# Kernel optimization log

Hardware: AMD Instinct MI355X
Metric: run time of the kernel (lower is better)

Reference implementation:

```python
import jax, jax.numpy as jnp
import numpy as np

NUM_HEADS = 8  # matches init_kwargs

def setup_inputs() -> dict:
    key = jax.random.key(0)
    ks = jax.random.split(key, 5)
    b, n, c = 8, 4096, 512
    scale_in = 1.0 / np.sqrt(c)
    return {
        'x': jax.random.normal(ks[0], (b, n, c), jnp.float32),
        'wqkv_w': jax.random.normal(ks[1], (3 * c, c), jnp.float32) * scale_in,
        'wqkv_b': jax.random.normal(ks[2], (3 * c,), jnp.float32) * 0.02,
        'wp_w': jax.random.normal(ks[3], (c, c), jnp.float32) * scale_in,
        'wp_b': jax.random.normal(ks[4], (c,), jnp.float32) * 0.02,
    }

def reference(x, wqkv_w, wqkv_b, wp_w, wp_b):
    b, n, c = x.shape
    h = NUM_HEADS
    d = c // h
    # QKV projection (torch Linear: x @ W^T + b)
    qkv = x @ wqkv_w.T + wqkv_b                      # (b, n, 3c)
    qkv = jnp.transpose(qkv.reshape(b, n, 3, c), (2, 0, 1, 3))
    q, k, v = qkv[0], qkv[1], qkv[2]                 # each (b, n, c)
    # Faithful to original: reshape (b,n,h,d) -> (b,h,n,d) is a FLAT
    # reinterpretation (torch .reshape), not a transpose.
    q = q.reshape(b, n, h, d).reshape(b, h, n, d)
    k = k.reshape(b, n, h, d).reshape(b, h, n, d)
    v = v.reshape(b, n, h, d).reshape(b, h, n, d)
    # Channel (cross-covariance) attention: contract over tokens n.
    scores = jnp.einsum('bhnd,bhne->bhde', q, k) / jnp.sqrt(jnp.float32(d))
    weights = jax.nn.softmax(scores, axis=-1)        # softmax over head_dim
    y = jnp.einsum('bhde,bhme->bhdm', weights, v)    # (b, h, d, n)
    y = jnp.transpose(y, (0, 3, 1, 2)).reshape(b, n, c)
    return y @ wp_w.T + wp_b
```

## Files before the change

kernel.cpp:

```cpp
#include <hip/hip_runtime.h>

typedef short s16x8 __attribute__((ext_vector_type(8)));
typedef float f32x4 __attribute__((ext_vector_type(4)));
typedef unsigned short us;

__device__ inline us f2bf(float f){
    union{float f;unsigned u;} v{f};
    unsigned r = v.u + 0x7fff + ((v.u>>16)&1);
    return (us)(r>>16);
}
__device__ inline float bf2f(us h){
    union{unsigned u;float f;} v{(unsigned)h<<16};
    return v.f;
}

__device__ __forceinline__ void glds16(const us* g, us* l){
    __builtin_amdgcn_global_load_lds(
        (const __attribute__((address_space(1))) unsigned int*)(g),
        (__attribute__((address_space(3))) unsigned int*)(l), 16, 0, 0);
}

__global__ void cast_f32_bf16(const float* __restrict__ src, us* __restrict__ dst, int n4){
    int i = blockIdx.x*blockDim.x + threadIdx.x;
    if(i < n4){
        float4 f = ((const float4*)src)[i];
        ushort4 o;
        o.x = f2bf(f.x); o.y = f2bf(f.y); o.z = f2bf(f.z); o.w = f2bf(f.w);
        ((ushort4*)dst)[i] = o;
    }
}

__launch_bounds__(256,2)
__global__ void gemm_qkv(const float* __restrict__ X, const us* __restrict__ B,
                         const float* __restrict__ bias, us* __restrict__ C){
    __shared__ __attribute__((aligned(16))) us sA[128*32];
    __shared__ __attribute__((aligned(16))) us sB[128*32];
    int t = threadIdx.x;
    int id = blockIdx.x;
    int xcd = id & 7, s = id >> 3;
    int nt = s % 12, mt = xcd*32 + s/12;
    int lane = t&63, wave = t>>6, quad = lane>>4, l15 = lane&15;
    int wm = wave>>1, wn = wave&1;

    int srA = t>>1, scA = (t&1)*16;
    const float* Ag = X + (size_t)(mt*128 + srA)*512 + scA;
    us* sAd = &sA[srA*32 + scA];

    int srB = wave*32 + (lane>>2), scB = (lane&3)*8;
    const us* Bg = B + (size_t)(nt*128 + srB)*512 + scB;
    us* sBw = &sB[(wave*32)*32];

    f32x4 acc[4][4];
    #pragma unroll
    for(int i=0;i<4;i++)
        #pragma unroll
        for(int j=0;j<4;j++) acc[i][j] = (f32x4){0.f,0.f,0.f,0.f};

    float4 p0 = ((const float4*)Ag)[0], p1 = ((const float4*)Ag)[1],
           p2 = ((const float4*)Ag)[2], p3 = ((const float4*)Ag)[3];

    for(int ki=0; ki<16; ki++){
        int k0 = ki*32;
        glds16(Bg + k0,          sBw);
        glds16(Bg + 16*512 + k0, sBw + 16*32);
        union{uint4 u[2]; us h[16];} o;
        o.h[0]=f2bf(p0.x); o.h[1]=f2bf(p0.y); o.h[2]=f2bf(p0.z); o.h[3]=f2bf(p0.w);
        o.h[4]=f2bf(p1.x); o.h[5]=f2bf(p1.y); o.h[6]=f2bf(p1.z); o.h[7]=f2bf(p1.w);
        o.h[8]=f2bf(p2.x); o.h[9]=f2bf(p2.y); o.h[10]=f2bf(p2.z); o.h[11]=f2bf(p2.w);
        o.h[12]=f2bf(p3.x); o.h[13]=f2bf(p3.y); o.h[14]=f2bf(p3.z); o.h[15]=f2bf(p3.w);
        *(uint4*)sAd = o.u[0]; *(uint4*)(sAd+8) = o.u[1];
        if(ki<15){
            const float4* nxt = (const float4*)(Ag + k0 + 32);
            p0 = nxt[0]; p1 = nxt[1]; p2 = nxt[2]; p3 = nxt[3];
        }
        __syncthreads();
        s16x8 af[4], bfr[4];
        #pragma unroll
        for(int i=0;i<4;i++) af[i]  = *(const s16x8*)&sA[(wm*64 + i*16 + l15)*32 + quad*8];
        #pragma unroll
        for(int j=0;j<4;j++) bfr[j] = *(const s16x8*)&sB[(wn*64 + j*16 + l15)*32 + quad*8];
        #pragma unroll
        for(int i=0;i<4;i++)
            #pragma unroll
            for(int j=0;j<4;j++)
                acc[i][j] = __builtin_amdgcn_mfma_f32_16x16x32_bf16(af[i], bfr[j], acc[i][j], 0,0,0);
        __syncthreads();
    }

    int row0 = mt*128 + wm*64, col0 = nt*128 + wn*64;
    #pragma unroll
    for(int j=0;j<4;j++){
        int col = col0 + j*16 + l15;
        float bv = bias[col];
        #pragma unroll
        for(int i=0;i<4;i++){
            int rbase = row0 + i*16 + quad*4;
            #pragma unroll
            for(int r=0;r<4;r++)
                C[(size_t)(rbase+r)*1536 + col] = f2bf(acc[i][j][r] + bv);
        }
    }
}

__launch_bounds__(256,2)
__global__ void attn_scores_mfma(const us* __restrict__ qkv, float* __restrict__ Sp){
    __shared__ __attribute__((aligned(16))) us sQt[64*64];
    __shared__ __attribute__((aligned(16))) us sKt[64*64];
    int t = threadIdx.x;
    int kb = blockIdx.x, head = blockIdx.y;
    int lane = t & 63, w = t >> 6;
    int quad = lane >> 4, l15 = lane & 15;

    f32x4 acc[4];
    #pragma unroll
    for(int j=0;j<4;j++) acc[j] = (f32x4){0.f,0.f,0.f,0.f};

    for(int chunk=0; chunk<8; chunk++){
        int r0 = head*512 + kb*64 + chunk*8;
        #pragma unroll
        for(int it=0; it<2; it++){
            int i = it*256 + t;
            int row8 = i>>6, l = i&63;
            int d0 = (l&7)*8;
            int off = ((row8 ^ (l&7))<<3) | (l>>3);
            const us* gq = qkv + (size_t)(r0+row8)*1536 + l*8;
            union{uint4 v; us s[8];} q, k;
            q.v = *(const uint4*)gq;
            k.v = *(const uint4*)(gq + 512);
            #pragma unroll
            for(int j=0;j<8;j++){
                sQt[(d0+j)*64 + off] = q.s[j];
                sKt[(d0+j)*64 + off] = k.s[j];
            }
        }
        __syncthreads();
        #pragma unroll
        for(int ks=0; ks<2; ks++){
            int d = w*16 + l15;
            int tb = ks*4 + quad;
            s16x8 af = *(const s16x8*)&sQt[d*64 + ((tb ^ (d>>3))<<3)];
            #pragma unroll
            for(int jt=0; jt<4; jt++){
                int e = jt*16 + l15;
                s16x8 bfv = *(const s16x8*)&sKt[e*64 + ((tb ^ (e>>3))<<3)];
                acc[jt] = __builtin_amdgcn_mfma_f32_16x16x32_bf16(af, bfv, acc[jt], 0,0,0);
            }
        }
        __syncthreads();
    }

    float* S = Sp + (size_t)(kb*64 + head)*4096;
    #pragma unroll
    for(int jt=0; jt<4; jt++){
        int e = jt*16 + l15;
        #pragma unroll
        for(int r=0; r<4; r++){
            int d = w*16 + quad*4 + r;
            S[d*64 + e] = acc[jt][r];
        }
    }
}

__global__ void softmax_fuse(const float* __restrict__ Sp, us* __restrict__ W){
    int head = blockIdx.x;
    int t = threadIdx.x;
    int d = t>>2, eg = (t&3)*16;
    float v[16];
    #pragma unroll
    for(int e=0;e<16;e++) v[e]=0.f;
    for(int kb=0; kb<8; kb++){
        const float* p = Sp + (size_t)(kb*64 + head)*4096 + d*64 + eg;
        #pragma unroll
        for(int e4=0;e4<4;e4++){
            float4 f = ((const float4*)p)[e4];
            v[e4*4+0]+=f.x; v[e4*4+1]+=f.y; v[e4*4+2]+=f.z; v[e4*4+3]+=f.w;
        }
    }
    float m = -1e30f;
    #pragma unroll
    for(int e=0;e<16;e++){ v[e] *= 0.125f; m = fmaxf(m, v[e]); }
    m = fmaxf(m, __shfl_xor(m, 1));
    m = fmaxf(m, __shfl_xor(m, 2));
    float s = 0.f;
    #pragma unroll
    for(int e=0;e<16;e++){ v[e] = __expf(v[e]-m); s += v[e]; }
    s += __shfl_xor(s, 1);
    s += __shfl_xor(s, 2);
    float inv = 1.f/s;
    union{uint4 u[2]; us h[16];} o;
    #pragma unroll
    for(int e=0;e<16;e++) o.h[e] = f2bf(v[e]*inv);
    uint4* wp = (uint4*)(W + (size_t)head*4096 + d*64 + eg);
    wp[0] = o.u[0]; wp[1] = o.u[1];
}

__launch_bounds__(256,1)
__global__ void wpfold(const us* __restrict__ wpbf, const us* __restrict__ W,
                       us* __restrict__ Mcat){
    __shared__ us sWt[64*72];
    int t = threadIdx.x;
    int head = blockIdx.x, b = head>>3, h = head&7;
    int lane = t&63, w = t>>6, quad = lane>>4, l15 = lane&15;
    #pragma unroll
    for(int it=0; it<2; it++){
        int idx = it*2048 + t*8;
        int d = idx>>6, e0 = idx&63;
        union{uint4 v; us s[8];} q;
        q.v = *(const uint4*)&W[(size_t)head*4096 + idx];
        #pragma unroll
        for(int j=0;j<8;j++) sWt[(e0+j)*72 + d] = q.s[j];
    }
    __syncthreads();
    #pragma unroll
    for(int i=0;i<8;i++){
        int nO = w*128 + i*16 + l15;
        s16x8 af0 = *(const s16x8*)&wpbf[(size_t)nO*512 + h*64 + quad*8];
        s16x8 af1 = *(const s16x8*)&wpbf[(size_t)nO*512 + h*64 + 32 + quad*8];
        #pragma unroll
        for(int j=0;j<4;j++){
            s16x8 bf0 = *(const s16x8*)&sWt[(j*16+l15)*72 + quad*8];
            s16x8 bf1 = *(const s16x8*)&sWt[(j*16+l15)*72 + 32 + quad*8];
            f32x4 acc = (f32x4){0.f,0.f,0.f,0.f};
            acc = __builtin_amdgcn_mfma_f32_16x16x32_bf16(af0, bf0, acc, 0,0,0);
            acc = __builtin_amdgcn_mfma_f32_16x16x32_bf16(af1, bf1, acc, 0,0,0);
            #pragma unroll
            for(int r=0;r<4;r++){
                int row = w*128 + i*16 + quad*4 + r;
                Mcat[((size_t)(b*512 + row))*512 + h*64 + j*16 + l15] = f2bf(acc[r]);
            }
        }
    }
}

__launch_bounds__(256,2)
__global__ void gemm_vout(const us* __restrict__ qkv, const us* __restrict__ Mcat,
                          const float* __restrict__ bias, float* __restrict__ out){
    __shared__ __attribute__((aligned(16))) us sA[128*32];
    __shared__ __attribute__((aligned(16))) us sB[128*32];
    int t = threadIdx.x;
    int id = blockIdx.x;
    int xcd = id & 7, s = id >> 3;
    int nt = s & 3, mt = xcd*32 + (s>>2);
    int b = mt>>5, mr = mt&31;
    int lane = t&63, wave = t>>6, quad = lane>>4, l15 = lane&15;
    int wm = wave>>1, wn = wave&1;

    int r = wave*32 + (lane>>2);
    int m = mr*128 + r;
    const us* Abase = qkv + ((size_t)(8*b)*512 + (m>>3))*1536 + 1024 + (m&7)*64 + (lane&3)*8;
    us* sAw = &sA[(wave*32)*32];

    int srB = wave*32 + (lane>>2), scB = (lane&3)*8;
    const us* Bg = Mcat + ((size_t)(b*512 + nt*128 + srB))*512 + scB;
    us* sBw = &sB[(wave*32)*32];

    f32x4 acc[4][4];
    #pragma unroll
    for(int i=0;i<4;i++)
        #pragma unroll
        for(int j=0;j<4;j++) acc[i][j] = (f32x4){0.f,0.f,0.f,0.f};

    for(int ki=0; ki<16; ki++){
        int k0 = ki*32;
        int h = k0>>6, e0 = k0&63;
        const us* Ag = Abase + (size_t)h*512*1536 + e0;
        glds16(Ag,            sAw);
        glds16(Ag + 2*1536,   sAw + 16*32);
        glds16(Bg + k0,           sBw);
        glds16(Bg + 16*512 + k0,  sBw + 16*32);
        __syncthreads();
        s16x8 af[4], bfr[4];
        #pragma unroll
        for(int i=0;i<4;i++) af[i]  = *(const s16x8*)&sA[(wm*64 + i*16 + l15)*32 + quad*8];
        #pragma unroll
        for(int j=0;j<4;j++) bfr[j] = *(const s16x8*)&sB[(wn*64 + j*16 + l15)*32 + quad*8];
        #pragma unroll
        for(int i=0;i<4;i++)
            #pragma unroll
            for(int j=0;j<4;j++)
                acc[i][j] = __builtin_amdgcn_mfma_f32_16x16x32_bf16(af[i], bfr[j], acc[i][j], 0,0,0);
        __syncthreads();
    }

    int row0 = b*4096 + mr*128 + wm*64;
    int col0 = nt*128 + wn*64;
    #pragma unroll
    for(int j=0;j<4;j++){
        int col = col0 + j*16 + l15;
        float bv = bias[col];
        #pragma unroll
        for(int i=0;i<4;i++){
            int rbase = row0 + i*16 + quad*4;
            #pragma unroll
            for(int r2=0;r2<4;r2++)
                out[(size_t)(rbase+r2)*512 + col] = acc[i][j][r2] + bv;
        }
    }
}

extern "C" void kernel_launch(void* const* d_in, const int* in_sizes, int n_in,
                              void* d_out, int out_size, void* d_ws, size_t ws_size,
                              hipStream_t stream){
    const float* x      = (const float*)d_in[0];
    const float* wqkv_w = (const float*)d_in[1];
    const float* wqkv_b = (const float*)d_in[2];
    const float* wp_w   = (const float*)d_in[3];
    const float* wp_b   = (const float*)d_in[4];

    char* ws = (char*)d_ws;
    us*    qkvbf  = (us*)(ws);
    float* Spart  = (float*)(ws + 100663296);
    us*    Wsm    = (us*)(ws + 109051904);
    us*    Mcat   = (us*)(ws + 109576192);
    us*    wqkvbf = (us*)(ws + 113770496);
    us*    wpbf   = (us*)(ws + 115343360);

    cast_f32_bf16<<<768, 256,0,stream>>>(wqkv_w, wqkvbf, 786432/4);
    cast_f32_bf16<<<256, 256,0,stream>>>(wp_w,   wpbf,   262144/4);

    gemm_qkv<<<3072,256,0,stream>>>(x, wqkvbf, wqkv_b, qkvbf);

    attn_scores_mfma<<<dim3(8,64),256,0,stream>>>(qkvbf, Spart);
    softmax_fuse<<<64,256,0,stream>>>(Spart, Wsm);

    wpfold<<<64,256,0,stream>>>(wpbf, Wsm, Mcat);

    gemm_vout<<<1024,256,0,stream>>>(qkvbf, Mcat, wp_b, (float*)d_out);
}
```

Before: 275.4 us.

## Pre-cast x to bf16, fuse softmax into fold, restage attention LDS loads

Adds a separate cast of x to bf16 so the QKV GEMM can stage both operands with direct global-to-LDS loads instead of converting fp32 in registers. Merges the two weight casts into one launch and folds the softmax kernel into the Wp-fold kernel, which removes a launch and the intermediate weights buffer. The score kernel's transposed LDS staging now uses padded rows with packed 32-bit stores in place of the XOR swizzle, and its occupancy bound is raised. In exchange it adds an extra pass over x (a read of fp32 and a write of bf16) through global memory.

```diff
diff --git a/kernel.cpp b/kernel.cpp
--- a/kernel.cpp
+++ b/kernel.cpp
@@ -9,10 +9,6 @@
     unsigned r = v.u + 0x7fff + ((v.u>>16)&1);
     return (us)(r>>16);
 }
-__device__ inline float bf2f(us h){
-    union{unsigned u;float f;} v{(unsigned)h<<16};
-    return v.f;
-}
 
 __device__ __forceinline__ void glds16(const us* g, us* l){
     __builtin_amdgcn_global_load_lds(
@@ -20,7 +16,7 @@
         (__attribute__((address_space(3))) unsigned int*)(l), 16, 0, 0);
 }
 
-__global__ void cast_f32_bf16(const float* __restrict__ src, us* __restrict__ dst, int n4){
+__global__ void cast_x(const float* __restrict__ src, us* __restrict__ dst, int n4){
     int i = blockIdx.x*blockDim.x + threadIdx.x;
     if(i < n4){
         float4 f = ((const float4*)src)[i];
@@ -30,8 +26,20 @@
     }
 }
 
+__global__ void cast_w(const float* __restrict__ wqkv_w, const float* __restrict__ wp_w,
+                       us* __restrict__ wqkvbf, us* __restrict__ wpbf){
+    int i = blockIdx.x*blockDim.x + threadIdx.x;
+    const float* s; us* d; int j;
+    if(i < 196608){ s = wqkv_w; d = wqkvbf; j = i; }
+    else          { s = wp_w;   d = wpbf;   j = i - 196608; }
+    float4 f = ((const float4*)s)[j];
+    ushort4 o;
+    o.x = f2bf(f.x); o.y = f2bf(f.y); o.z = f2bf(f.z); o.w = f2bf(f.w);
+    ((ushort4*)d)[j] = o;
+}
+
 __launch_bounds__(256,2)
-__global__ void gemm_qkv(const float* __restrict__ X, const us* __restrict__ B,
+__global__ void gemm_qkv(const us* __restrict__ A, const us* __restrict__ B,
                          const float* __restrict__ bias, us* __restrict__ C){
     __shared__ __attribute__((aligned(16))) us sA[128*32];
     __shared__ __attribute__((aligned(16))) us sB[128*32];
@@ -42,12 +50,11 @@
     int lane = t&63, wave = t>>6, quad = lane>>4, l15 = lane&15;
     int wm = wave>>1, wn = wave&1;
 
-    int srA = t>>1, scA = (t&1)*16;
-    const float* Ag = X + (size_t)(mt*128 + srA)*512 + scA;
-    us* sAd = &sA[srA*32 + scA];
-
-    int srB = wave*32 + (lane>>2), scB = (lane&3)*8;
-    const us* Bg = B + (size_t)(nt*128 + srB)*512 + scB;
+    int srow = wave*32 + (lane>>2);
+    int scol = (lane&3)*8;
+    const us* Ag = A + (size_t)(mt*128 + srow)*512 + scol;
+    const us* Bg = B + (size_t)(nt*128 + srow)*512 + scol;
+    us* sAw = &sA[(wave*32)*32];
     us* sBw = &sB[(wave*32)*32];
 
     f32x4 acc[4][4];
@@ -56,23 +63,11 @@
         #pragma unroll
         for(int j=0;j<4;j++) acc[i][j] = (f32x4){0.f,0.f,0.f,0.f};
 
-    float4 p0 = ((const float4*)Ag)[0], p1 = ((const float4*)Ag)[1],
-           p2 = ((const float4*)Ag)[2], p3 = ((const float4*)Ag)[3];
-
-    for(int ki=0; ki<16; ki++){
-        int k0 = ki*32;
+    for(int k0=0; k0<512; k0+=32){
+        glds16(Ag + k0,          sAw);
+        glds16(Ag + 16*512 + k0, sAw + 16*32);
         glds16(Bg + k0,          sBw);
         glds16(Bg + 16*512 + k0, sBw + 16*32);
-        union{uint4 u[2]; us h[16];} o;
-        o.h[0]=f2bf(p0.x); o.h[1]=f2bf(p0.y); o.h[2]=f2bf(p0.z); o.h[3]=f2bf(p0.w);
-        o.h[4]=f2bf(p1.x); o.h[5]=f2bf(p1.y); o.h[6]=f2bf(p1.z); o.h[7]=f2bf(p1.w);
-        o.h[8]=f2bf(p2.x); o.h[9]=f2bf(p2.y); o.h[10]=f2bf(p2.z); o.h[11]=f2bf(p2.w);
-        o.h[12]=f2bf(p3.x); o.h[13]=f2bf(p3.y); o.h[14]=f2bf(p3.z); o.h[15]=f2bf(p3.w);
-        *(uint4*)sAd = o.u[0]; *(uint4*)(sAd+8) = o.u[1];
-        if(ki<15){
-            const float4* nxt = (const float4*)(Ag + k0 + 32);
-            p0 = nxt[0]; p1 = nxt[1]; p2 = nxt[2]; p3 = nxt[3];
-        }
         __syncthreads();
         s16x8 af[4], bfr[4];
         #pragma unroll
@@ -102,14 +97,16 @@
     }
 }
 
-__launch_bounds__(256,2)
+__launch_bounds__(256,4)
 __global__ void attn_scores_mfma(const us* __restrict__ qkv, float* __restrict__ Sp){
-    __shared__ __attribute__((aligned(16))) us sQt[64*64];
-    __shared__ __attribute__((aligned(16))) us sKt[64*64];
+    __shared__ __attribute__((aligned(16))) us sQt[64*72];
+    __shared__ __attribute__((aligned(16))) us sKt[64*72];
     int t = threadIdx.x;
     int kb = blockIdx.x, head = blockIdx.y;
     int lane = t & 63, w = t >> 6;
     int quad = lane >> 4, l15 = lane & 15;
+    int p = t & 31;
+    int d0 = (t >> 5) * 8;
 
     f32x4 acc[4];
     #pragma unroll
@@ -117,32 +114,25 @@
 
     for(int chunk=0; chunk<8; chunk++){
         int r0 = head*512 + kb*64 + chunk*8;
-        #pragma unroll
-        for(int it=0; it<2; it++){
-            int i = it*256 + t;
-            int row8 = i>>6, l = i&63;
-            int d0 = (l&7)*8;
-            int off = ((row8 ^ (l&7))<<3) | (l>>3);
-            const us* gq = qkv + (size_t)(r0+row8)*1536 + l*8;
-            union{uint4 v; us s[8];} q, k;
-            q.v = *(const uint4*)gq;
-            k.v = *(const uint4*)(gq + 512);
-            #pragma unroll
-            for(int j=0;j<8;j++){
-                sQt[(d0+j)*64 + off] = q.s[j];
-                sKt[(d0+j)*64 + off] = k.s[j];
-            }
-        }
-        __syncthreads();
+        const us* g = qkv + (size_t)(r0 + (p>>2))*1536 + (2*(p&3))*64 + d0;
+        union{uint4 v; us h[8];} q0, q1, k0, k1;
+        q0.v = *(const uint4*)g;         q1.v = *(const uint4*)(g + 64);
+        k0.v = *(const uint4*)(g + 512); k1.v = *(const uint4*)(g + 576);
+        #pragma unroll
+        for(int j=0;j<8;j++){
+            *(unsigned*)&sQt[(d0+j)*72 + 2*p] = (unsigned)q0.h[j] | ((unsigned)q1.h[j]<<16);
+            *(unsigned*)&sKt[(d0+j)*72 + 2*p] = (unsigned)k0.h[j] | ((unsigned)k1.h[j]<<16);
+        }
+        __syncthreads();
+        int d = w*16 + l15;
         #pragma unroll
         for(int ks=0; ks<2; ks++){
-            int d = w*16 + l15;
             int tb = ks*4 + quad;
-            s16x8 af = *(const s16x8*)&sQt[d*64 + ((tb ^ (d>>3))<<3)];
+            s16x8 af = *(const s16x8*)&sQt[d*72 + tb*8];
             #pragma unroll
             for(int jt=0; jt<4; jt++){
                 int e = jt*16 + l15;
-                s16x8 bfv = *(const s16x8*)&sKt[e*64 + ((tb ^ (e>>3))<<3)];
+                s16x8 bfv = *(const s16x8*)&sKt[e*72 + tb*8];
                 acc[jt] = __builtin_amdgcn_mfma_f32_16x16x32_bf16(af, bfv, acc[jt], 0,0,0);
             }
         }
@@ -161,56 +151,43 @@
     }
 }
 
-__global__ void softmax_fuse(const float* __restrict__ Sp, us* __restrict__ W){
-    int head = blockIdx.x;
-    int t = threadIdx.x;
-    int d = t>>2, eg = (t&3)*16;
-    float v[16];
-    #pragma unroll
-    for(int e=0;e<16;e++) v[e]=0.f;
-    for(int kb=0; kb<8; kb++){
-        const float* p = Sp + (size_t)(kb*64 + head)*4096 + d*64 + eg;
-        #pragma unroll
-        for(int e4=0;e4<4;e4++){
-            float4 f = ((const float4*)p)[e4];
-            v[e4*4+0]+=f.x; v[e4*4+1]+=f.y; v[e4*4+2]+=f.z; v[e4*4+3]+=f.w;
-        }
-    }
-    float m = -1e30f;
-    #pragma unroll
-    for(int e=0;e<16;e++){ v[e] *= 0.125f; m = fmaxf(m, v[e]); }
-    m = fmaxf(m, __shfl_xor(m, 1));
-    m = fmaxf(m, __shfl_xor(m, 2));
-    float s = 0.f;
-    #pragma unroll
-    for(int e=0;e<16;e++){ v[e] = __expf(v[e]-m); s += v[e]; }
-    s += __shfl_xor(s, 1);
-    s += __shfl_xor(s, 2);
-    float inv = 1.f/s;
-    union{uint4 u[2]; us h[16];} o;
-    #pragma unroll
-    for(int e=0;e<16;e++) o.h[e] = f2bf(v[e]*inv);
-    uint4* wp = (uint4*)(W + (size_t)head*4096 + d*64 + eg);
-    wp[0] = o.u[0]; wp[1] = o.u[1];
-}
-
 __launch_bounds__(256,1)
-__global__ void wpfold(const us* __restrict__ wpbf, const us* __restrict__ W,
+__global__ void smfold(const float* __restrict__ Sp, const us* __restrict__ wpbf,
                        us* __restrict__ Mcat){
     __shared__ us sWt[64*72];
     int t = threadIdx.x;
     int head = blockIdx.x, b = head>>3, h = head&7;
     int lane = t&63, w = t>>6, quad = lane>>4, l15 = lane&15;
-    #pragma unroll
-    for(int it=0; it<2; it++){
-        int idx = it*2048 + t*8;
-        int d = idx>>6, e0 = idx&63;
-        union{uint4 v; us s[8];} q;
-        q.v = *(const uint4*)&W[(size_t)head*4096 + idx];
-        #pragma unroll
-        for(int j=0;j<8;j++) sWt[(e0+j)*72 + d] = q.s[j];
+
+    {
+        int d = t>>2, eg = (t&3)*16;
+        float v[16];
+        #pragma unroll
+        for(int e=0;e<16;e++) v[e]=0.f;
+        for(int kb=0; kb<8; kb++){
+            const float* pp = Sp + (size_t)(kb*64 + head)*4096 + d*64 + eg;
+            #pragma unroll
+            for(int e4=0;e4<4;e4++){
+                float4 f = ((const float4*)pp)[e4];
+                v[e4*4+0]+=f.x; v[e4*4+1]+=f.y; v[e4*4+2]+=f.z; v[e4*4+3]+=f.w;
+            }
+        }
+        float m = -1e30f;
+        #pragma unroll
+        for(int e=0;e<16;e++){ v[e] *= 0.125f; m = fmaxf(m, v[e]); }
+        m = fmaxf(m, __shfl_xor(m, 1));
+        m = fmaxf(m, __shfl_xor(m, 2));
+        float s = 0.f;
+        #pragma unroll
+        for(int e=0;e<16;e++){ v[e] = __expf(v[e]-m); s += v[e]; }
+        s += __shfl_xor(s, 1);
+        s += __shfl_xor(s, 2);
+        float inv = 1.f/s;
+        #pragma unroll
+        for(int e=0;e<16;e++) sWt[(eg+e)*72 + d] = f2bf(v[e]*inv);
     }
     __syncthreads();
+
     #pragma unroll
     for(int i=0;i<8;i++){
         int nO = w*128 + i*16 + l15;
@@ -309,21 +286,20 @@
 
     char* ws = (char*)d_ws;
     us*    qkvbf  = (us*)(ws);
-    float* Spart  = (float*)(ws + 100663296);
-    us*    Wsm    = (us*)(ws + 109051904);
-    us*    Mcat   = (us*)(ws + 109576192);
-    us*    wqkvbf = (us*)(ws + 113770496);
-    us*    wpbf   = (us*)(ws + 115343360);
-
-    cast_f32_bf16<<<768, 256,0,stream>>>(wqkv_w, wqkvbf, 786432/4);
-    cast_f32_bf16<<<256, 256,0,stream>>>(wp_w,   wpbf,   262144/4);
-
-    gemm_qkv<<<3072,256,0,stream>>>(x, wqkvbf, wqkv_b, qkvbf);
+    us*    xbf    = (us*)(ws + 100663296);
+    float* Spart  = (float*)(ws + 134217728);
+    us*    Mcat   = (us*)(ws + 142606336);
+    us*    wqkvbf = (us*)(ws + 146800640);
+    us*    wpbf   = (us*)(ws + 148373504);
+
+    cast_w<<<1024,256,0,stream>>>(wqkv_w, wp_w, wqkvbf, wpbf);
+    cast_x<<<16384,256,0,stream>>>(x, xbf, 16777216/4);
+
+    gemm_qkv<<<3072,256,0,stream>>>(xbf, wqkvbf, wqkv_b, qkvbf);
 
     attn_scores_mfma<<<dim3(8,64),256,0,stream>>>(qkvbf, Spart);
-    softmax_fuse<<<64,256,0,stream>>>(Spart, Wsm);
-
-    wpfold<<<64,256,0,stream>>>(wpbf, Wsm, Mcat);
+
+    smfold<<<64,256,0,stream>>>(Spart, wpbf, Mcat);
 
     gemm_vout<<<1024,256,0,stream>>>(qkvbf, Mcat, wp_b, (float*)d_out);
 }
```

Measured after the change: 252.3 us. 1.09x faster.
